# Kernel tuning notes

Hardware: AMD Instinct MI355X
Metric: run time of the kernel (lower is better)

Reference implementation:

```python
import jax, jax.numpy as jnp
import numpy as np


def _fir_kernel():
    # StyleGAN-2 low-pass FIR: outer([1,3,3,1]) normalized to sum 1
    k1 = jnp.array([1.0, 3.0, 3.0, 1.0], dtype=jnp.float32)
    k2 = jnp.outer(k1, k1)
    return k2 / k2.sum()


def setup_inputs() -> dict:
    key = jax.random.key(0)
    kx, kw = jax.random.split(key, 2)
    B, H, W, C, OC = 8, 128, 128, 128, 128
    x = jax.random.normal(kx, (B, H, W, C), dtype=jnp.float32)
    conv_w = jax.random.normal(kw, (3, 3, C, OC), dtype=jnp.float32) * 0.02  # HWIO
    conv_b = jnp.zeros((OC,), dtype=jnp.float32)
    return {"x": x, "conv_w": conv_w, "conv_b": conv_b}


def _upsample_fir(x):
    B, H, W, C = x.shape
    kernel = _fir_kernel()
    x_up = jnp.zeros((B, 2 * H, 2 * W, C), dtype=x.dtype)
    x_up = x_up.at[:, ::2, ::2, :].set(x)
    k = jnp.tile(kernel[None, None, :, :], (C, 1, 1, 1))  # OIHW, O=C, I=1
    y = jax.lax.conv_general_dilated(
        jnp.transpose(x_up, (0, 3, 1, 2)),  # NCHW
        k * 4.0,
        window_strides=(1, 1),
        padding="SAME",
        feature_group_count=C,
    )
    return jnp.transpose(y, (0, 2, 3, 1))  # back to NHWC


def reference(x, conv_w, conv_b):
    x_up = _upsample_fir(x)  # (B, 2H, 2W, C)
    out = jax.lax.conv_general_dilated(
        x_up,
        conv_w,
        window_strides=(1, 1),
        padding="SAME",
        dimension_numbers=("NHWC", "HWIO", "NHWC"),
    )
    return out + conv_b
```

## Files before the change

### kernel.cpp

```cpp
#include <hip/hip_runtime.h>

typedef __bf16 bf16x8 __attribute__((ext_vector_type(8)));
typedef float f32x4 __attribute__((ext_vector_type(4)));
typedef unsigned short ushort8 __attribute__((ext_vector_type(8)));

__device__ __forceinline__ unsigned short f2bf(float f) {
  unsigned int u = __builtin_bit_cast(unsigned int, f);
  u += 0x7FFFu + ((u >> 16) & 1u);
  return (unsigned short)(u >> 16);
}

__constant__ float COEF[2][3][3] = {
    {{0.25f, 0.00f, 0.00f},
     {0.75f, 0.75f, 0.25f},
     {0.00f, 0.25f, 0.75f}},
    {{0.75f, 0.25f, 0.00f},
     {0.25f, 0.75f, 0.75f},
     {0.00f, 0.00f, 0.25f}}
};

__global__ void pack_weights(const float* __restrict__ w, unsigned short* __restrict__ pw) {
  const int kt = blockIdx.x >> 3, nt = blockIdx.x & 7;
  const int l = threadIdx.x;
  const int tap = kt >> 2, cblk = kt & 3;
  const int du = tap / 3, dv = tap - du * 3;
  const int c0 = cblk * 32 + ((l >> 4) << 3);
  const int oc = nt * 16 + (l & 15);
  float accp[4][8];
#pragma unroll
  for (int ph = 0; ph < 4; ++ph)
#pragma unroll
    for (int j = 0; j < 8; ++j) accp[ph][j] = 0.0f;
#pragma unroll
  for (int u = 0; u < 3; ++u)
#pragma unroll
    for (int v = 0; v < 3; ++v) {
      const float ra0 = COEF[0][du][u], ra1 = COEF[1][du][u];
      const float cb0 = COEF[0][dv][v], cb1 = COEF[1][dv][v];
      const float c00 = ra0 * cb0, c01 = ra0 * cb1, c10 = ra1 * cb0, c11 = ra1 * cb1;
#pragma unroll
      for (int j = 0; j < 8; ++j) {
        const float wv = w[((u * 3 + v) * 128 + c0 + j) * 128 + oc];
        accp[0][j] += c00 * wv;
        accp[1][j] += c01 * wv;
        accp[2][j] += c10 * wv;
        accp[3][j] += c11 * wv;
      }
    }
  const int fi = ((cblk * 3 + dv) * 3 + du) * 8 + nt;
#pragma unroll
  for (int ph = 0; ph < 4; ++ph) {
    ushort8 o;
#pragma unroll
    for (int j = 0; j < 8; ++j) o[j] = f2bf(accp[ph][j]);
    *(ushort8*)(pw + (((ph * 288 + fi) * 64 + l) << 3)) = o;
  }
}

__global__ __launch_bounds__(512, 2) void fused_all(
    const float* __restrict__ x, const unsigned short* __restrict__ pw,
    const float* __restrict__ w, const float* __restrict__ bias,
    float* __restrict__ out) {
  __shared__ __align__(16) char smem[11 * 19 * 256];

  const int bid = blockIdx.x;
  const int tid = threadIdx.x;

  if (bid < 512) {
    const int chunk = bid & 31;
    const int type = (bid >> 5) & 1;
    const int bi = bid >> 6;
    const int base0 = chunk * 8;
    const float* xb = x + bi * (128 * 128 * 128);

    float* yw = (float*)smem;
    float* part = (float*)(smem + 16384);

    {
      const int c = tid & 127;
      const int sub = tid >> 7;
      for (int k = sub; k < 20; k += 4) {
        const int f = k / 10;
        const int ws = k - f * 10;
        const int t = base0 - 1 + ws;
        float val = 0.0f;
        if ((unsigned)t < 256u) {
          const int t0 = t >> 1;
          const float hA0 = (t & 1) ? 0.25f : 0.75f;
          const float hA1 = 1.0f - hA0;
          const float hF0 = f ? 0.25f : 0.75f;
          const float hF1 = 1.0f - hF0;
          const bool ok = (t0 + 1) < 128;
          if (type == 0) {
            const float v00 = xb[t0 * 128 + c];
            const float v01 = ok ? xb[(t0 + 1) * 128 + c] : 0.0f;
            const float v10 = xb[(128 + t0) * 128 + c];
            const float v11 = ok ? xb[(128 + t0 + 1) * 128 + c] : 0.0f;
            val = hF0 * (hA0 * v00 + hA1 * v01) + hF1 * (hA0 * v10 + hA1 * v11);
          } else {
            const float v00 = xb[(t0 * 128) * 128 + c];
            const float v01 = xb[(t0 * 128 + 1) * 128 + c];
            const float v10 = ok ? xb[((t0 + 1) * 128) * 128 + c] : 0.0f;
            const float v11 = ok ? xb[((t0 + 1) * 128 + 1) * 128 + c] : 0.0f;
            val = hA0 * (hF0 * v00 + hF1 * v01) + hA1 * (hF0 * v10 + hF1 * v11);
          }
        }
        yw[(f * 10 + ws) * 128 + c] = val;
      }
    }
    __syncthreads();

    const int wv = tid >> 6;
    const int oc0 = (tid & 63) * 2;
    const int cbase = wv * 16;

    float acc[8][2] = {};
#pragma unroll 1
    for (int cc = 0; cc < 16; ++cc) {
      float yr[2][10];
#pragma unroll
      for (int f = 0; f < 2; ++f)
#pragma unroll
        for (int ws = 0; ws < 10; ++ws)
          yr[f][ws] = yw[(f * 10 + ws) * 128 + cbase + cc];
#pragma unroll
      for (int tf = 0; tf < 2; ++tf) {
#pragma unroll
        for (int tb = 0; tb < 3; ++tb) {
          const int uu = (type == 0) ? (tf + 1) : tb;
          const int vv = (type == 0) ? tb : (tf + 1);
          const float2 w2 = *(const float2*)(
              w + ((uu * 3 + vv) * 128 + cbase + cc) * 128 + oc0);
#pragma unroll
          for (int pos = 0; pos < 8; ++pos) {
            const float yv = yr[tf][pos + tb];
            acc[pos][0] += yv * w2.x;
            acc[pos][1] += yv * w2.y;
          }
        }
      }
    }

#pragma unroll
    for (int pos = 0; pos < 8; ++pos)
      *(float2*)(part + (wv * 8 + pos) * 128 + oc0) = *(float2*)acc[pos];
    __syncthreads();

    const int pos = tid >> 6;
    const int ocp = (tid & 63) * 2;
    float s0 = 0.0f, s1 = 0.0f;
#pragma unroll
    for (int w8 = 0; w8 < 8; ++w8) {
      const float2 v = *(const float2*)(part + (w8 * 8 + pos) * 128 + ocp);
      s0 += v.x; s1 += v.y;
    }
    const int posg = base0 + pos;
    if (!(type == 1 && posg == 0)) {
      const int p = (type == 0) ? 0 : posg;
      const int q = (type == 0) ? posg : 0;
      const float2 b2 = *(const float2*)(bias + ocp);
      float2 r; r.x = s0 + b2.x; r.y = s1 + b2.y;
      *(float2*)(out + bi * (256 * 256 * 128) + (p * 256 + q) * 128 + ocp) = r;
    }
    return;
  }

  char* xlds = smem;
  const int o = bid - 512;
  const int blk = (o & 7) * 128 + (o >> 3);
  const int bimg = blk >> 7;
  const int it = (blk >> 3) & 15;
  const int jt = blk & 7;
  const int I0 = it * 8, J0 = jt * 16;
  const float* xb = x + bimg * (128 * 128 * 128);

  const int lane = tid & 63;
  const int l15 = lane & 15;
  const int lh = lane >> 4;
  const int wid = tid >> 6;
  const int a = (wid >> 2) & 1;
  const int b = (wid >> 1) & 1;
  const int nhalf = wid & 1;
  const int ph = a * 2 + b;

  const char* pwb = (const char*)pw + ph * 294912 + nhalf * 4096 + lane * 16;

#define LOADB(buf, g_, du_)                                           \
  do {                                                                \
    const char* bp_ = pwb + (((g_) * 3 + (du_)) << 13);               \
    _Pragma("unroll") for (int n = 0; n < 4; ++n)                     \
        buf[n] = *(const bf16x8*)(bp_ + n * 1024);                    \
  } while (0)

  bf16x8 b0[4], b1[4], b2[4];
  LOADB(b0, 0, 0);

  for (int idx = tid; idx < 11 * 19 * 16; idx += 512) {
    const int cp = idx & 15;
    const int pos = idx >> 4;
    const int xr = pos / 19;
    const int xc = pos - xr * 19;
    const int gi = I0 - 1 + xr;
    const int gj = J0 - 1 + xc;
    ushort8 u8 = {};
    if (((unsigned)gi < 128u) && ((unsigned)gj < 128u)) {
      const float* p = xb + ((gi << 7) + gj) * 128 + (cp << 3);
      const float4 A = *(const float4*)p;
      const float4 Bv = *(const float4*)(p + 4);
      u8[0] = f2bf(A.x); u8[1] = f2bf(A.y); u8[2] = f2bf(A.z); u8[3] = f2bf(A.w);
      u8[4] = f2bf(Bv.x); u8[5] = f2bf(Bv.y); u8[6] = f2bf(Bv.z); u8[7] = f2bf(Bv.w);
    }
    int byte = (pos << 8) + (cp << 4);
    byte ^= (pos & 7) << 4;
    *(ushort8*)(xlds + byte) = u8;
  }
  __syncthreads();

  f32x4 acc[8][4] = {};
  const int colpart = l15 + b;

#pragma unroll 1
  for (int g = 0; g < 12; ++g) {
    const int cblk = (g * 11) >> 5;
    const int dv = g - cblk * 3;
    const int kbyte = (cblk * 4 + lh) << 4;
    const int pbase = a * 19 + colpart + dv;

    bf16x8 af[10];
#define AREAD(rr)                                                     \
    do {                                                              \
      const int posa = pbase + (rr) * 19;                             \
      int byte_ = (posa << 8) + kbyte;                                \
      byte_ ^= (posa & 7) << 4;                \
      af[rr] = *(const bf16x8*)(xlds + byte_);                        \
    } while (0)

    AREAD(0); AREAD(1); AREAD(2); AREAD(3);
    AREAD(4); AREAD(5); AREAD(6); AREAD(7);
    LOADB(b1, g, 1);
    AREAD(8); AREAD(9);
    LOADB(b2, g, 2);

    __builtin_amdgcn_s_setprio(1);
#pragma unroll
    for (int m = 0; m < 8; ++m)
#pragma unroll
      for (int n = 0; n < 4; ++n)
        acc[m][n] = __builtin_amdgcn_mfma_f32_16x16x32_bf16(af[m], b0[n], acc[m][n], 0, 0, 0);
    __builtin_amdgcn_s_setprio(0);

    {
      const int gn = (g < 11) ? (g + 1) : 11;
      LOADB(b0, gn, 0);
    }

    __builtin_amdgcn_s_setprio(1);
#pragma unroll
    for (int m = 0; m < 8; ++m)
#pragma unroll
      for (int n = 0; n < 4; ++n)
        acc[m][n] = __builtin_amdgcn_mfma_f32_16x16x32_bf16(af[m + 1], b1[n], acc[m][n], 0, 0, 0);

#pragma unroll
    for (int m = 0; m < 8; ++m)
#pragma unroll
      for (int n = 0; n < 4; ++n)
        acc[m][n] = __builtin_amdgcn_mfma_f32_16x16x32_bf16(af[m + 2], b2[n], acc[m][n], 0, 0, 0);
    __builtin_amdgcn_s_setprio(0);
#undef AREAD
  }
#undef LOADB

  float bv[4];
#pragma unroll
  for (int n = 0; n < 4; ++n) bv[n] = bias[nhalf * 64 + n * 16 + l15];
  float* ob = out + bimg * (256 * 256 * 128) + nhalf * 64 + l15;
#pragma unroll
  for (int m = 0; m < 8; ++m) {
    const int p = it * 16 + 2 * m + a;
    if (p == 0) continue;
#pragma unroll
    for (int jr = 0; jr < 4; ++jr) {
      const int q = jt * 32 + 2 * (lh * 4 + jr) + b;
      if (q == 0) continue;
      float* orow = ob + (p * 256 + q) * 128;
#pragma unroll
      for (int n = 0; n < 4; ++n) orow[n * 16] = acc[m][n][jr] + bv[n];
    }
  }
}

extern "C" void kernel_launch(void* const* d_in, const int* in_sizes, int n_in,
                              void* d_out, int out_size, void* d_ws, size_t ws_size,
                              hipStream_t stream) {
  const float* x = (const float*)d_in[0];
  const float* w = (const float*)d_in[1];
  const float* bias = (const float*)d_in[2];
  float* out = (float*)d_out;
  unsigned short* pw = (unsigned short*)d_ws;

  pack_weights<<<dim3(288), dim3(64), 0, stream>>>(w, pw);
  fused_all<<<dim3(1536), dim3(512), 0, stream>>>(x, pw, w, bias, out);
}
```

Baseline: 172.1 us.

## Pre-convert input to bf16 and double-buffer LDS tiles via async global-to-LDS loads

```diff
diff --git a/kernel.cpp b/kernel.cpp
--- a/kernel.cpp
+++ b/kernel.cpp
@@ -57,19 +57,36 @@
   }
 }
 
-__global__ __launch_bounds__(512, 2) void fused_all(
+__global__ void precvt(const float* __restrict__ x, unsigned short* __restrict__ xbf) {
+  const int i = blockIdx.x * 256 + threadIdx.x;
+  for (int it8 = i; it8 < 2097152; it8 += 524288) {
+    const float* p = x + (long long)it8 * 8;
+    const float4 A = *(const float4*)p;
+    const float4 B = *(const float4*)(p + 4);
+    ushort8 o;
+    o[0] = f2bf(A.x); o[1] = f2bf(A.y); o[2] = f2bf(A.z); o[3] = f2bf(A.w);
+    o[4] = f2bf(B.x); o[5] = f2bf(B.y); o[6] = f2bf(B.z); o[7] = f2bf(B.w);
+    *(ushort8*)(xbf + (long long)it8 * 8) = o;
+  }
+  if (blockIdx.x == 0 && threadIdx.x < 8)
+    ((unsigned long long*)(xbf + 16777216))[threadIdx.x] = 0ULL;
+}
+
+__global__ __launch_bounds__(512, 2) void fused_main(
     const float* __restrict__ x, const unsigned short* __restrict__ pw,
-    const float* __restrict__ w, const float* __restrict__ bias,
-    float* __restrict__ out) {
-  __shared__ __align__(16) char smem[11 * 19 * 256];
+    const unsigned short* __restrict__ xbf, const float* __restrict__ w,
+    const float* __restrict__ bias, float* __restrict__ out,
+    const unsigned short* __restrict__ zp) {
+  __shared__ __align__(16) char smem[2 * 54272];
 
   const int bid = blockIdx.x;
   const int tid = threadIdx.x;
 
-  if (bid < 512) {
-    const int chunk = bid & 31;
-    const int type = (bid >> 5) & 1;
-    const int bi = bid >> 6;
+  if (bid >= 256) {
+    const int bb = bid - 256;
+    const int chunk = bb & 31;
+    const int type = (bb >> 5) & 1;
+    const int bi = bb >> 6;
     const int base0 = chunk * 8;
     const float* xb = x + bi * (128 * 128 * 128);
 
@@ -166,13 +183,13 @@
   }
 
   char* xlds = smem;
-  const int o = bid - 512;
-  const int blk = (o & 7) * 128 + (o >> 3);
-  const int bimg = blk >> 7;
-  const int it = (blk >> 3) & 15;
-  const int jt = blk & 7;
-  const int I0 = it * 8, J0 = jt * 16;
-  const float* xb = x + bimg * (128 * 128 * 128);
+  const int o = bid;
+  const int blk = (o & 7) * 32 + (o >> 3);
+  const int bimg = blk >> 5;
+  const int it = (blk >> 1) & 15;
+  const int jthalf = blk & 1;
+  const int I0 = it * 8;
+  const char* xbfb = (const char*)(xbf + bimg * (128 * 128 * 128));
 
   const int lane = tid & 63;
   const int l15 = lane & 15;
@@ -192,9 +209,243 @@
         buf[n] = *(const bf16x8*)(bp_ + n * 1024);                    \
   } while (0)
 
+#define STAGE(tt, wrbase)                                                        \
+  do {                                                                           \
+    const int J0n = (jthalf * 4 + (tt)) * 16;                                    \
+    for (int item = wid; item < 53; item += 8) {                                 \
+      const int p_ = item * 4 + (lane >> 4);                                     \
+      const int xr_ = p_ / 19;                                                   \
+      const int xc_ = p_ - xr_ * 19;                                             \
+      const int gi_ = I0 - 1 + xr_;                                              \
+      const int gj_ = J0n - 1 + xc_;                                             \
+      const int slot_ = (lane & 15) ^ (p_ & 15);                                 \
+      const char* src_;                                                          \
+      if (((unsigned)gi_ < 128u) && ((unsigned)gj_ < 128u) && (p_ < 209))        \
+        src_ = xbfb + (((gi_ << 7) + gj_) << 8) + (slot_ << 4);                  \
+      else                                                                       \
+        src_ = (const char*)zp;                                                  \
+      __builtin_amdgcn_global_load_lds(                                          \
+          (const __attribute__((address_space(1))) unsigned int*)src_,           \
+          (__attribute__((address_space(3))) unsigned int*)((wrbase) + item * 1024), \
+          16, 0, 0);                                                             \
+    }                                                                            \
+  } while (0)
+
+#define AREAD(rr, dv_, tq_)                                           \
+  do {                                                                \
+    const int posa = (a + (rr)) * 19 + colpart + (dv_);               \
+    const int byte_ = (posa << 8) + (((tq_) ^ (posa & 15)) << 4);     \
+    af[rr] = *(const bf16x8*)(rdbase + byte_);                        \
+  } while (0)
+
+#define MFMAS(du_, buf)                                               \
+  do {                                                                \
+    __builtin_amdgcn_s_setprio(1);                                    \
+    _Pragma("unroll") for (int m = 0; m < 8; ++m)                     \
+        _Pragma("unroll") for (int n = 0; n < 4; ++n)                 \
+            acc[m][n] = __builtin_amdgcn_mfma_f32_16x16x32_bf16(      \
+                af[(du_) + m], buf[n], acc[m][n], 0, 0, 0);           \
+    __builtin_amdgcn_s_setprio(0);                                    \
+  } while (0)
+
   bf16x8 b0[4], b1[4], b2[4];
   LOADB(b0, 0, 0);
-
+  STAGE(0, xlds);
+  __syncthreads();
+
+  float bv[4];
+#pragma unroll
+  for (int n = 0; n < 4; ++n) bv[n] = bias[nhalf * 64 + n * 16 + l15];
+  float* ob = out + bimg * (256 * 256 * 128) + nhalf * 64 + l15;
+  const int colpart = l15 + b;
+
+  f32x4 acc[8][4] = {};
+
+#pragma unroll 1
+  for (int t = 0; t < 4; ++t) {
+    const char* rdbase = xlds + (t & 1) * 54272;
+    char* wrbase = xlds + ((t & 1) ^ 1) * 54272;
+    if (t < 3) STAGE(t + 1, wrbase);
+
+#pragma unroll 1
+    for (int g = 0; g < 12; ++g) {
+      const int cblk = (g * 11) >> 5;
+      const int dv = g - cblk * 3;
+      const int tq = cblk * 4 + lh;
+
+      bf16x8 af[10];
+      AREAD(0, dv, tq); AREAD(1, dv, tq); AREAD(2, dv, tq); AREAD(3, dv, tq);
+      AREAD(4, dv, tq); AREAD(5, dv, tq); AREAD(6, dv, tq); AREAD(7, dv, tq);
+      LOADB(b1, g, 1);
+      AREAD(8, dv, tq); AREAD(9, dv, tq);
+      LOADB(b2, g, 2);
+
+      MFMAS(0, b0);
+      {
+        const int gn = (g < 11) ? (g + 1) : 0;
+        LOADB(b0, gn, 0);
+      }
+      MFMAS(1, b1);
+      MFMAS(2, b2);
+    }
+    __syncthreads();
+
+    const int jt = jthalf * 4 + t;
+#pragma unroll
+    for (int m = 0; m < 8; ++m) {
+      const int p = it * 16 + 2 * m + a;
+      if (p == 0) { 
+#pragma unroll
+        for (int n = 0; n < 4; ++n) acc[m][n] = (f32x4){0.f, 0.f, 0.f, 0.f};
+        continue;
+      }
+#pragma unroll
+      for (int jr = 0; jr < 4; ++jr) {
+        const int q = jt * 32 + 2 * (lh * 4 + jr) + b;
+        if (q == 0) continue;
+        float* orow = ob + (p * 256 + q) * 128;
+#pragma unroll
+        for (int n = 0; n < 4; ++n) orow[n * 16] = acc[m][n][jr] + bv[n];
+      }
+#pragma unroll
+      for (int n = 0; n < 4; ++n) acc[m][n] = (f32x4){0.f, 0.f, 0.f, 0.f};
+    }
+  }
+#undef AREAD
+#undef MFMAS
+#undef LOADB
+#undef STAGE
+}
+
+__global__ __launch_bounds__(512, 2) void fused_fb(
+    const float* __restrict__ x, const unsigned short* __restrict__ pw,
+    const float* __restrict__ w, const float* __restrict__ bias,
+    float* __restrict__ out) {
+  __shared__ __align__(16) char smem[11 * 19 * 256];
+
+  const int bid = blockIdx.x;
+  const int tid = threadIdx.x;
+
+  if (bid < 512) {
+    const int chunk = bid & 31;
+    const int type = (bid >> 5) & 1;
+    const int bi = bid >> 6;
+    const int base0 = chunk * 8;
+    const float* xb = x + bi * (128 * 128 * 128);
+    float* yw = (float*)smem;
+    float* part = (float*)(smem + 16384);
+    {
+      const int c = tid & 127;
+      const int sub = tid >> 7;
+      for (int k = sub; k < 20; k += 4) {
+        const int f = k / 10;
+        const int ws = k - f * 10;
+        const int t = base0 - 1 + ws;
+        float val = 0.0f;
+        if ((unsigned)t < 256u) {
+          const int t0 = t >> 1;
+          const float hA0 = (t & 1) ? 0.25f : 0.75f;
+          const float hA1 = 1.0f - hA0;
+          const float hF0 = f ? 0.25f : 0.75f;
+          const float hF1 = 1.0f - hF0;
+          const bool ok = (t0 + 1) < 128;
+          if (type == 0) {
+            const float v00 = xb[t0 * 128 + c];
+            const float v01 = ok ? xb[(t0 + 1) * 128 + c] : 0.0f;
+            const float v10 = xb[(128 + t0) * 128 + c];
+            const float v11 = ok ? xb[(128 + t0 + 1) * 128 + c] : 0.0f;
+            val = hF0 * (hA0 * v00 + hA1 * v01) + hF1 * (hA0 * v10 + hA1 * v11);
+          } else {
+            const float v00 = xb[(t0 * 128) * 128 + c];
+            const float v01 = xb[(t0 * 128 + 1) * 128 + c];
+            const float v10 = ok ? xb[((t0 + 1) * 128) * 128 + c] : 0.0f;
+            const float v11 = ok ? xb[((t0 + 1) * 128 + 1) * 128 + c] : 0.0f;
+            val = hA0 * (hF0 * v00 + hF1 * v01) + hA1 * (hF0 * v10 + hF1 * v11);
+          }
+        }
+        yw[(f * 10 + ws) * 128 + c] = val;
+      }
+    }
+    __syncthreads();
+    const int wv = tid >> 6;
+    const int oc0 = (tid & 63) * 2;
+    const int cbase = wv * 16;
+    float acc[8][2] = {};
+#pragma unroll 1
+    for (int cc = 0; cc < 16; ++cc) {
+      float yr[2][10];
+#pragma unroll
+      for (int f = 0; f < 2; ++f)
+#pragma unroll
+        for (int ws = 0; ws < 10; ++ws)
+          yr[f][ws] = yw[(f * 10 + ws) * 128 + cbase + cc];
+#pragma unroll
+      for (int tf = 0; tf < 2; ++tf) {
+#pragma unroll
+        for (int tb = 0; tb < 3; ++tb) {
+          const int uu = (type == 0) ? (tf + 1) : tb;
+          const int vv = (type == 0) ? tb : (tf + 1);
+          const float2 w2 = *(const float2*)(
+              w + ((uu * 3 + vv) * 128 + cbase + cc) * 128 + oc0);
+#pragma unroll
+          for (int pos = 0; pos < 8; ++pos) {
+            const float yv = yr[tf][pos + tb];
+            acc[pos][0] += yv * w2.x;
+            acc[pos][1] += yv * w2.y;
+          }
+        }
+      }
+    }
+#pragma unroll
+    for (int pos = 0; pos < 8; ++pos)
+      *(float2*)(part + (wv * 8 + pos) * 128 + oc0) = *(float2*)acc[pos];
+    __syncthreads();
+    const int pos = tid >> 6;
+    const int ocp = (tid & 63) * 2;
+    float s0 = 0.0f, s1 = 0.0f;
+#pragma unroll
+    for (int w8 = 0; w8 < 8; ++w8) {
+      const float2 v = *(const float2*)(part + (w8 * 8 + pos) * 128 + ocp);
+      s0 += v.x; s1 += v.y;
+    }
+    const int posg = base0 + pos;
+    if (!(type == 1 && posg == 0)) {
+      const int p = (type == 0) ? 0 : posg;
+      const int q = (type == 0) ? posg : 0;
+      const float2 b2 = *(const float2*)(bias + ocp);
+      float2 r; r.x = s0 + b2.x; r.y = s1 + b2.y;
+      *(float2*)(out + bi * (256 * 256 * 128) + (p * 256 + q) * 128 + ocp) = r;
+    }
+    return;
+  }
+
+  char* xlds = smem;
+  const int o = bid - 512;
+  const int blk = (o & 7) * 128 + (o >> 3);
+  const int bimg = blk >> 7;
+  const int it = (blk >> 3) & 15;
+  const int jt = blk & 7;
+  const int I0 = it * 8, J0 = jt * 16;
+  const float* xb = x + bimg * (128 * 128 * 128);
+  const int lane = tid & 63;
+  const int l15 = lane & 15;
+  const int lh = lane >> 4;
+  const int wid = tid >> 6;
+  const int a = (wid >> 2) & 1;
+  const int b = (wid >> 1) & 1;
+  const int nhalf = wid & 1;
+  const int ph = a * 2 + b;
+  const char* pwb = (const char*)pw + ph * 294912 + nhalf * 4096 + lane * 16;
+
+#define LOADBF(buf, g_, du_)                                          \
+  do {                                                                \
+    const char* bp_ = pwb + (((g_) * 3 + (du_)) << 13);               \
+    _Pragma("unroll") for (int n = 0; n < 4; ++n)                     \
+        buf[n] = *(const bf16x8*)(bp_ + n * 1024);                    \
+  } while (0)
+
+  bf16x8 b0[4], b1[4], b2[4];
+  LOADBF(b0, 0, 0);
   for (int idx = tid; idx < 11 * 19 * 16; idx += 512) {
     const int cp = idx & 15;
     const int pos = idx >> 4;
@@ -215,62 +466,47 @@
     *(ushort8*)(xlds + byte) = u8;
   }
   __syncthreads();
-
   f32x4 acc[8][4] = {};
   const int colpart = l15 + b;
-
+#define AREADF(rr)                                                    \
+    do {                                                              \
+      const int posa = pbase + (rr) * 19;                             \
+      int byte_ = (posa << 8) + kbyte;                                \
+      byte_ ^= (posa & 7) << 4;                                       \
+      af[rr] = *(const bf16x8*)(xlds + byte_);                        \
+    } while (0)
+#define MFMASF(du_, buf)                                              \
+  do {                                                                \
+    __builtin_amdgcn_s_setprio(1);                                    \
+    _Pragma("unroll") for (int m = 0; m < 8; ++m)                     \
+        _Pragma("unroll") for (int n = 0; n < 4; ++n)                 \
+            acc[m][n] = __builtin_amdgcn_mfma_f32_16x16x32_bf16(      \
+                af[(du_) + m], buf[n], acc[m][n], 0, 0, 0);           \
+    __builtin_amdgcn_s_setprio(0);                                    \
+  } while (0)
 #pragma unroll 1
   for (int g = 0; g < 12; ++g) {
     const int cblk = (g * 11) >> 5;
     const int dv = g - cblk * 3;
     const int kbyte = (cblk * 4 + lh) << 4;
     const int pbase = a * 19 + colpart + dv;
-
     bf16x8 af[10];
-#define AREAD(rr)                                                     \
-    do {                                                              \
-      const int posa = pbase + (rr) * 19;                             \
-      int byte_ = (posa << 8) + kbyte;                                \
-      byte_ ^= (posa & 7) << 4;                \
-      af[rr] = *(const bf16x8*)(xlds + byte_);                        \
-    } while (0)
-
-    AREAD(0); AREAD(1); AREAD(2); AREAD(3);
-    AREAD(4); AREAD(5); AREAD(6); AREAD(7);
-    LOADB(b1, g, 1);
-    AREAD(8); AREAD(9);
-    LOADB(b2, g, 2);
-
-    __builtin_amdgcn_s_setprio(1);
-#pragma unroll
-    for (int m = 0; m < 8; ++m)
-#pragma unroll
-      for (int n = 0; n < 4; ++n)
-        acc[m][n] = __builtin_amdgcn_mfma_f32_16x16x32_bf16(af[m], b0[n], acc[m][n], 0, 0, 0);
-    __builtin_amdgcn_s_setprio(0);
-
+    AREADF(0); AREADF(1); AREADF(2); AREADF(3);
+    AREADF(4); AREADF(5); AREADF(6); AREADF(7);
+    LOADBF(b1, g, 1);
+    AREADF(8); AREADF(9);
+    LOADBF(b2, g, 2);
+    MFMASF(0, b0);
     {
       const int gn = (g < 11) ? (g + 1) : 11;
-      LOADB(b0, gn, 0);
-    }
-
-    __builtin_amdgcn_s_setprio(1);
-#pragma unroll
-    for (int m = 0; m < 8; ++m)
-#pragma unroll
-      for (int n = 0; n < 4; ++n)
-        acc[m][n] = __builtin_amdgcn_mfma_f32_16x16x32_bf16(af[m + 1], b1[n], acc[m][n], 0, 0, 0);
-
-#pragma unroll
-    for (int m = 0; m < 8; ++m)
-#pragma unroll
-      for (int n = 0; n < 4; ++n)
-        acc[m][n] = __builtin_amdgcn_mfma_f32_16x16x32_bf16(af[m + 2], b2[n], acc[m][n], 0, 0, 0);
-    __builtin_amdgcn_s_setprio(0);
-#undef AREAD
-  }
-#undef LOADB
-
+      LOADBF(b0, gn, 0);
+    }
+    MFMASF(1, b1);
+    MFMASF(2, b2);
+  }
+#undef AREADF
+#undef MFMASF
+#undef LOADBF
   float bv[4];
 #pragma unroll
   for (int n = 0; n < 4; ++n) bv[n] = bias[nhalf * 64 + n * 16 + l15];
@@ -298,7 +534,15 @@
   const float* bias = (const float*)d_in[2];
   float* out = (float*)d_out;
   unsigned short* pw = (unsigned short*)d_ws;
+  unsigned short* xbf = (unsigned short*)((char*)d_ws + 1179648);
+  const unsigned short* zp = xbf + 16777216;
+  const size_t NEED = 1179648ull + 33554432ull + 64ull;
 
   pack_weights<<<dim3(288), dim3(64), 0, stream>>>(w, pw);
-  fused_all<<<dim3(1536), dim3(512), 0, stream>>>(x, pw, w, bias, out);
+  if (ws_size >= NEED) {
+    precvt<<<dim3(2048), dim3(256), 0, stream>>>(x, xbf);
+    fused_main<<<dim3(768), dim3(512), 0, stream>>>(x, pw, xbf, w, bias, out, zp);
+  } else {
+    fused_fb<<<dim3(1536), dim3(512), 0, stream>>>(x, pw, w, bias, out);
+  }
 }
```

After: 194.4 us. +12.9%, slower.

## Make GEMM blocks loop over four column tiles and reorder block dispatch

Applied to the files above, without the earlier changes.

```diff
diff --git a/kernel.cpp b/kernel.cpp
--- a/kernel.cpp
+++ b/kernel.cpp
@@ -66,10 +66,11 @@
   const int bid = blockIdx.x;
   const int tid = threadIdx.x;
 
-  if (bid < 512) {
-    const int chunk = bid & 31;
-    const int type = (bid >> 5) & 1;
-    const int bi = bid >> 6;
+  if (bid >= 256) {
+    const int bb = bid - 256;
+    const int chunk = bb & 31;
+    const int type = (bb >> 5) & 1;
+    const int bi = bb >> 6;
     const int base0 = chunk * 8;
     const float* xb = x + bi * (128 * 128 * 128);
 
@@ -166,12 +167,12 @@
   }
 
   char* xlds = smem;
-  const int o = bid - 512;
-  const int blk = (o & 7) * 128 + (o >> 3);
-  const int bimg = blk >> 7;
-  const int it = (blk >> 3) & 15;
-  const int jt = blk & 7;
-  const int I0 = it * 8, J0 = jt * 16;
+  const int o = bid;
+  const int blk = (o & 7) * 32 + (o >> 3);
+  const int bimg = blk >> 5;
+  const int it = (blk >> 1) & 15;
+  const int jh = blk & 1;
+  const int I0 = it * 8;
   const float* xb = x + bimg * (128 * 128 * 128);
 
   const int lane = tid & 63;
@@ -192,102 +193,104 @@
         buf[n] = *(const bf16x8*)(bp_ + n * 1024);                    \
   } while (0)
 
-  bf16x8 b0[4], b1[4], b2[4];
-  LOADB(b0, 0, 0);
-
-  for (int idx = tid; idx < 11 * 19 * 16; idx += 512) {
-    const int cp = idx & 15;
-    const int pos = idx >> 4;
-    const int xr = pos / 19;
-    const int xc = pos - xr * 19;
-    const int gi = I0 - 1 + xr;
-    const int gj = J0 - 1 + xc;
-    ushort8 u8 = {};
-    if (((unsigned)gi < 128u) && ((unsigned)gj < 128u)) {
-      const float* p = xb + ((gi << 7) + gj) * 128 + (cp << 3);
-      const float4 A = *(const float4*)p;
-      const float4 Bv = *(const float4*)(p + 4);
-      u8[0] = f2bf(A.x); u8[1] = f2bf(A.y); u8[2] = f2bf(A.z); u8[3] = f2bf(A.w);
-      u8[4] = f2bf(Bv.x); u8[5] = f2bf(Bv.y); u8[6] = f2bf(Bv.z); u8[7] = f2bf(Bv.w);
-    }
-    int byte = (pos << 8) + (cp << 4);
-    byte ^= (pos & 7) << 4;
-    *(ushort8*)(xlds + byte) = u8;
-  }
-  __syncthreads();
-
-  f32x4 acc[8][4] = {};
-  const int colpart = l15 + b;
-
-#pragma unroll 1
-  for (int g = 0; g < 12; ++g) {
-    const int cblk = (g * 11) >> 5;
-    const int dv = g - cblk * 3;
-    const int kbyte = (cblk * 4 + lh) << 4;
-    const int pbase = a * 19 + colpart + dv;
-
-    bf16x8 af[10];
-#define AREAD(rr)                                                     \
+#define AREADP(rr)                                                    \
     do {                                                              \
       const int posa = pbase + (rr) * 19;                             \
       int byte_ = (posa << 8) + kbyte;                                \
-      byte_ ^= (posa & 7) << 4;                \
+      byte_ ^= (posa & 7) << 4;                                       \
       af[rr] = *(const bf16x8*)(xlds + byte_);                        \
     } while (0)
 
-    AREAD(0); AREAD(1); AREAD(2); AREAD(3);
-    AREAD(4); AREAD(5); AREAD(6); AREAD(7);
-    LOADB(b1, g, 1);
-    AREAD(8); AREAD(9);
-    LOADB(b2, g, 2);
-
-    __builtin_amdgcn_s_setprio(1);
-#pragma unroll
-    for (int m = 0; m < 8; ++m)
-#pragma unroll
-      for (int n = 0; n < 4; ++n)
-        acc[m][n] = __builtin_amdgcn_mfma_f32_16x16x32_bf16(af[m], b0[n], acc[m][n], 0, 0, 0);
-    __builtin_amdgcn_s_setprio(0);
-
-    {
-      const int gn = (g < 11) ? (g + 1) : 11;
-      LOADB(b0, gn, 0);
-    }
-
-    __builtin_amdgcn_s_setprio(1);
-#pragma unroll
-    for (int m = 0; m < 8; ++m)
-#pragma unroll
-      for (int n = 0; n < 4; ++n)
-        acc[m][n] = __builtin_amdgcn_mfma_f32_16x16x32_bf16(af[m + 1], b1[n], acc[m][n], 0, 0, 0);
-
-#pragma unroll
-    for (int m = 0; m < 8; ++m)
-#pragma unroll
-      for (int n = 0; n < 4; ++n)
-        acc[m][n] = __builtin_amdgcn_mfma_f32_16x16x32_bf16(af[m + 2], b2[n], acc[m][n], 0, 0, 0);
-    __builtin_amdgcn_s_setprio(0);
-#undef AREAD
-  }
-#undef LOADB
+#define MFMASP(du_, buf)                                              \
+  do {                                                                \
+    __builtin_amdgcn_s_setprio(1);                                    \
+    _Pragma("unroll") for (int m = 0; m < 8; ++m)                     \
+        _Pragma("unroll") for (int n = 0; n < 4; ++n)                 \
+            acc[m][n] = __builtin_amdgcn_mfma_f32_16x16x32_bf16(      \
+                af[(du_) + m], buf[n], acc[m][n], 0, 0, 0);           \
+    __builtin_amdgcn_s_setprio(0);                                    \
+  } while (0)
+
+  bf16x8 b0[4], b1[4], b2[4];
+  LOADB(b0, 0, 0);
 
   float bv[4];
 #pragma unroll
   for (int n = 0; n < 4; ++n) bv[n] = bias[nhalf * 64 + n * 16 + l15];
   float* ob = out + bimg * (256 * 256 * 128) + nhalf * 64 + l15;
-#pragma unroll
-  for (int m = 0; m < 8; ++m) {
-    const int p = it * 16 + 2 * m + a;
-    if (p == 0) continue;
-#pragma unroll
-    for (int jr = 0; jr < 4; ++jr) {
-      const int q = jt * 32 + 2 * (lh * 4 + jr) + b;
-      if (q == 0) continue;
-      float* orow = ob + (p * 256 + q) * 128;
-#pragma unroll
-      for (int n = 0; n < 4; ++n) orow[n * 16] = acc[m][n][jr] + bv[n];
+  const int colpart = l15 + b;
+
+  f32x4 acc[8][4] = {};
+
+#pragma unroll 1
+  for (int t = 0; t < 4; ++t) {
+    const int jt = jh * 4 + t;
+    const int J0 = jt * 16;
+
+    if (t > 0) __syncthreads();
+
+    for (int idx = tid; idx < 11 * 19 * 16; idx += 512) {
+      const int cp = idx & 15;
+      const int pos = idx >> 4;
+      const int xr = pos / 19;
+      const int xc = pos - xr * 19;
+      const int gi = I0 - 1 + xr;
+      const int gj = J0 - 1 + xc;
+      ushort8 u8 = {};
+      if (((unsigned)gi < 128u) && ((unsigned)gj < 128u)) {
+        const float* p = xb + ((gi << 7) + gj) * 128 + (cp << 3);
+        const float4 A = *(const float4*)p;
+        const float4 Bv = *(const float4*)(p + 4);
+        u8[0] = f2bf(A.x); u8[1] = f2bf(A.y); u8[2] = f2bf(A.z); u8[3] = f2bf(A.w);
+        u8[4] = f2bf(Bv.x); u8[5] = f2bf(Bv.y); u8[6] = f2bf(Bv.z); u8[7] = f2bf(Bv.w);
+      }
+      int byte = (pos << 8) + (cp << 4);
+      byte ^= (pos & 7) << 4;
+      *(ushort8*)(xlds + byte) = u8;
+    }
+    __syncthreads();
+
+#pragma unroll 1
+    for (int g = 0; g < 12; ++g) {
+      const int cblk = (g * 11) >> 5;
+      const int dv = g - cblk * 3;
+      const int kbyte = (cblk * 4 + lh) << 4;
+      const int pbase = a * 19 + colpart + dv;
+      bf16x8 af[10];
+      AREADP(0); AREADP(1); AREADP(2); AREADP(3);
+      AREADP(4); AREADP(5); AREADP(6); AREADP(7);
+      LOADB(b1, g, 1);
+      AREADP(8); AREADP(9);
+      LOADB(b2, g, 2);
+      MFMASP(0, b0);
+      {
+        const int gn = (g < 11) ? (g + 1) : 0;
+        LOADB(b0, gn, 0);
+      }
+      MFMASP(1, b1);
+      MFMASP(2, b2);
+    }
+
+#pragma unroll
+    for (int m = 0; m < 8; ++m) {
+      const int p = it * 16 + 2 * m + a;
+      if (p != 0) {
+#pragma unroll
+        for (int jr = 0; jr < 4; ++jr) {
+          const int q = jt * 32 + 2 * (lh * 4 + jr) + b;
+          if (q == 0) continue;
+          float* orow = ob + (p * 256 + q) * 128;
+#pragma unroll
+          for (int n = 0; n < 4; ++n) orow[n * 16] = acc[m][n][jr] + bv[n];
+        }
+      }
+#pragma unroll
+      for (int n = 0; n < 4; ++n) acc[m][n] = (f32x4){0.f, 0.f, 0.f, 0.f};
     }
   }
+#undef AREADP
+#undef MFMASP
+#undef LOADB
 }
 
 extern "C" void kernel_launch(void* const* d_in, const int* in_sizes, int n_in,
@@ -300,5 +303,5 @@
   unsigned short* pw = (unsigned short*)d_ws;
 
   pack_weights<<<dim3(288), dim3(64), 0, stream>>>(w, pw);
-  fused_all<<<dim3(1536), dim3(512), 0, stream>>>(x, pw, w, bias, out);
+  fused_all<<<dim3(768), dim3(512), 0, stream>>>(x, pw, w, bias, out);
 }
```

New measurement: 169.7 us. No clear change (-1.4%).
